# Performance work log

Measured on AMD Instinct MI355X. Metric: run time of the kernel, lower is better.

The kernel has to match this reference:

```python
import jax, jax.numpy as jnp
import numpy as np

N = 20000
F_IN = 500
HID = 64
CLS = 16
H = 4
K_KNN = 10
NEG_SLOPE = 0.2


def _edges(key, n_rand):
    # random edges plus self-loops (mirrors add_self_loops in the torch code)
    src = jax.random.randint(key, (n_rand,), 0, N)
    dst = jax.random.randint(jax.random.fold_in(key, 1), (n_rand,), 0, N)
    loops = jnp.arange(N)
    return jnp.stack([jnp.concatenate([src, loops]), jnp.concatenate([dst, loops])]).astype(jnp.int32)


def setup_inputs():
    key = jax.random.key(0)
    ks = jax.random.split(key, 40)
    inp = {}
    inp['x'] = jax.random.normal(ks[0], (N, F_IN), jnp.float32)
    inp['edge_index_1'] = _edges(ks[1], 16 * N)          # 1-hop graph, 340k edges
    inp['edge_index_2'] = _edges(ks[2], 32 * N)          # denser 2-hop graph, 660k edges
    knn_src = jnp.repeat(jnp.arange(N), K_KNN)
    knn_dst = jax.random.randint(ks[3], (K_KNN * N,), 0, N)
    inp['edge_index_knn'] = jnp.stack([knn_src, knn_dst]).astype(jnp.int32)

    def p(k, shape):
        return jax.random.normal(k, shape, jnp.float32) * 0.05

    dims = {1: (F_IN, HID), 2: (HID, CLS), 3: (F_IN, HID), 4: (HID, CLS), 5: (F_IN, HID), 6: (HID, CLS)}
    i = 4
    for j in range(1, 7):
        fi, fo = dims[j]
        inp[f'W{j}'] = p(ks[i], (fi, H, fo)); i += 1
        inp[f'as{j}'] = p(ks[i], (H, fo)); i += 1
        inp[f'ad{j}'] = p(ks[i], (H, fo)); i += 1
        inp[f'b{j}'] = jnp.zeros((fo,), jnp.float32)
    for j in range(1, 4):
        inp[f'lin{j}_w'] = p(ks[i], (CLS, CLS)); i += 1
        inp[f'lin{j}_b'] = jnp.zeros((CLS,), jnp.float32)
    inp['agg_w'] = p(ks[i], (CLS,))
    return inp


def gat_conv(x, ei, W, a_s, a_d, b):
    # PyG GATConv, concat=False (mean over heads). W: [F,H,D], a_s/a_d: [H,D], b: [D]
    src, dst = ei[0], ei[1]
    z = jnp.einsum('nf,fhd->nhd', x, W)                 # [N,H,D]
    e_src = jnp.sum(z * a_s, -1)                         # [N,H]
    e_dst = jnp.sum(z * a_d, -1)                         # [N,H]
    e = jax.nn.leaky_relu(e_src[src] + e_dst[dst], NEG_SLOPE)   # [E,H]
    m = jax.ops.segment_max(e, dst, num_segments=N)      # per-dst softmax (edge softmax)
    p = jnp.exp(e - m[dst])
    s = jax.ops.segment_sum(p, dst, num_segments=N)
    alpha = p / (s[dst] + 1e-16)                         # [E,H]
    out = jax.ops.segment_sum(alpha[:, :, None] * z[src], dst, num_segments=N)  # [N,H,D]
    return out.mean(1) + b


def reference(x, edge_index_1, edge_index_2, edge_index_knn,
              W1, as1, ad1, b1, W2, as2, ad2, b2,
              W3, as3, ad3, b3, W4, as4, ad4, b4,
              W5, as5, ad5, b5, W6, as6, ad6, b6,
              lin1_w, lin1_b, lin2_w, lin2_b, lin3_w, lin3_b, agg_w):
    # eval mode: dropout is a no-op
    h1 = jax.nn.relu(gat_conv(x, edge_index_1, W1, as1, ad1, b1))
    h1 = gat_conv(h1, edge_index_1, W2, as2, ad2, b2)
    h2 = jax.nn.relu(gat_conv(x, edge_index_2, W3, as3, ad3, b3))
    h2 = gat_conv(h2, edge_index_2, W4, as4, ad4, b4)
    h3 = jax.nn.relu(gat_conv(x, edge_index_knn, W5, as5, ad5, b5))
    h3 = gat_conv(h3, edge_index_knn, W6, as6, ad6, b6)

    a1 = jnp.tanh(h1 @ lin1_w + lin1_b) @ agg_w          # [N]
    a2 = jnp.tanh(h2 @ lin2_w + lin2_b) @ agg_w
    a3 = jnp.tanh(h3 @ lin3_w + lin3_b) @ agg_w
    a = jax.nn.softmax(jnp.stack([a1, a2, a3], axis=1), axis=1)  # [N,3]
    h = a[:, 0:1] * h1 + a[:, 1:2] * h2 + a[:, 2:3] * h3
    return jax.nn.log_softmax(h, axis=1)
```

## Files before the change

kernel.cpp:

```cpp
#include <hip/hip_runtime.h>
#include <hip/hip_bf16.h>
#include <math.h>

#define N_NODES 20000
#define MP      20096
#define FIN     500
#define KP      512
#define NBUCK   157

typedef unsigned short u16;
typedef unsigned char  u8;
typedef __attribute__((ext_vector_type(8))) short   short8;
typedef __attribute__((ext_vector_type(2))) unsigned uv2;
typedef __attribute__((ext_vector_type(2))) float   f32x2;
typedef __attribute__((ext_vector_type(4))) float   f32x4;

__device__ __forceinline__ float b2f(u16 u){
  union { unsigned int i; float f; } v; v.i = ((unsigned int)u) << 16; return v.f;
}
__device__ __forceinline__ u16 f2b(float f){
  __hip_bfloat16 h = __float2bfloat16(f);
  return *reinterpret_cast<u16*>(&h);
}
__device__ __forceinline__ float lrelu(float x){ return x >= 0.f ? x : 0.2f * x; }
__device__ __forceinline__ float ldp(const void* p, int i, int bf){
  return bf ? b2f(((const u16*)p)[i]) : ((const float*)p)[i];
}
__device__ __forceinline__ u8 f2fp8(float f){
  return (u8)(__builtin_amdgcn_cvt_pk_fp8_f32(f, 0.f, 0, false) & 0xff);
}
template<bool HI>
__device__ __forceinline__ f32x2 fp8pair(unsigned w){
  return __builtin_amdgcn_cvt_pk_f32_fp8((int)w, HI);
}
__device__ __forceinline__ void gll16(const u16* g, u16* l){
  __builtin_amdgcn_global_load_lds(
      (const __attribute__((address_space(1))) unsigned int*)g,
      (__attribute__((address_space(3))) unsigned int*)l, 16, 0, 0);
}
__device__ __forceinline__ void barrier_lgkm(){
  asm volatile("s_waitcnt lgkmcnt(0)" ::: "memory");
  __builtin_amdgcn_s_barrier();
  asm volatile("" ::: "memory");
}

__global__ __launch_bounds__(1024) void detect_dtype_kernel(const unsigned int* __restrict__ xw, int nwords,
                                                            int* __restrict__ flag){
  __shared__ int cnt;
  if (threadIdx.x == 0) cnt = 0;
  __syncthreads();
  int c = 0;
  for (int i = threadIdx.x; i < nwords; i += 1024){
    unsigned e = (xw[i] >> 7) & 0xFF;
    if (e >= 0x70 && e <= 0x8F) c++;
  }
  atomicAdd(&cnt, c);
  __syncthreads();
  if (threadIdx.x == 0) *flag = (cnt * 2 > nwords) ? 1 : 0;
}

#define CHA 8192
#define PB  1024
__global__ __launch_bounds__(PB) void prep_kernel(
    const void* __restrict__ x, u16* __restrict__ xp,
    const void* Wb0, const void* Wb1, const void* Wb2,
    const void* Ws0, const void* Ws1, const void* Ws2,
    u16* ob0, u16* ob1, u16* ob2, u16* os0, u16* os1, u16* os2,
    const int* s0, const int* s1, const int* s2,
    const int* d0, const int* d1, const int* d2,
    int E0, int E1, int E2, int S0, int S1, int S2, int EB,
    int* __restrict__ bucketCur, unsigned* p0, unsigned* p1, unsigned* p2,
    const int* __restrict__ flag){
  __shared__ int hb[NBUCK];
  __shared__ int loff[NBUCK];
  __shared__ int hbase[NBUCK];
  __shared__ unsigned shp[CHA];
  __shared__ u8 shb[CHA];
  __shared__ u16 tile[64][65];
  int bf = *flag;
  int tid = threadIdx.x;
  if (blockIdx.y == 0){
    int t = blockIdx.x * PB + tid;
    if (t >= MP * 64) return;
    int row = t >> 6;
    int j0  = (t & 63) * 8;
    short8 v = {0,0,0,0,0,0,0,0};
    if (row < N_NODES){
      if (j0 + 8 <= FIN){
        if (bf){
          const ushort4* xr = (const ushort4*)((const u16*)x + (size_t)row * FIN + j0);
          ushort4 a = xr[0], b = xr[1];
          v[0]=(short)a.x; v[1]=(short)a.y; v[2]=(short)a.z; v[3]=(short)a.w;
          v[4]=(short)b.x; v[5]=(short)b.y; v[6]=(short)b.z; v[7]=(short)b.w;
        } else {
          const float4* xr = (const float4*)((const float*)x + (size_t)row * FIN + j0);
          float4 a = xr[0], b = xr[1];
          v[0]=(short)f2b(a.x); v[1]=(short)f2b(a.y); v[2]=(short)f2b(a.z); v[3]=(short)f2b(a.w);
          v[4]=(short)f2b(b.x); v[5]=(short)f2b(b.y); v[6]=(short)f2b(b.z); v[7]=(short)f2b(b.w);
        }
      } else {
#pragma unroll
        for (int j = 0; j < 8; ++j){
          int k = j0 + j;
          u16 val = 0;
          if (k < FIN)
            val = bf ? ((const u16*)x)[(size_t)row * FIN + k]
                     : f2b(((const float*)x)[(size_t)row * FIN + k]);
          v[j] = (short)val;
        }
      }
    }
    *(short8*)(xp + (size_t)row * KP + j0) = v;
  } else if (blockIdx.y == 1){
    int xb = blockIdx.x;
    if (xb >= 96 + 3) return;
    int tx = tid & 63, tyb = tid >> 6;
    const void* Wsrc; u16* O; int SRCW, SRCH, DSTW, kt, nt;
    if (xb < 96){
      int which = xb >> 5, tl = xb & 31;
      nt = (tl & 3) << 6; kt = (tl >> 2) << 6;
      Wsrc = which == 0 ? Wb0 : (which == 1 ? Wb1 : Wb2);
      O    = which == 0 ? ob0 : (which == 1 ? ob1 : ob2);
      SRCW = 256; SRCH = FIN; DSTW = KP;
    } else {
      int which = xb - 96;
      nt = 0; kt = 0;
      Wsrc = which == 0 ? Ws0 : (which == 1 ? Ws1 : Ws2);
      O    = which == 0 ? os0 : (which == 1 ? os1 : os2);
      SRCW = 64; SRCH = 64; DSTW = 64;
    }
#pragma unroll
    for (int r = 0; r < 4; ++r){
      int kl = tyb + r * 16;
      int k = kt + kl, n = nt + tx;
      u16 vv = 0;
      if (k < SRCH)
        vv = bf ? ((const u16*)Wsrc)[(size_t)k * SRCW + n]
                : f2b(((const float*)Wsrc)[(size_t)k * SRCW + n]);
      tile[kl][tx] = vv;
    }
    __syncthreads();
#pragma unroll
    for (int r = 0; r < 4; ++r){
      int nl = tyb + r * 16;
      O[(size_t)(nt + nl) * DSTW + kt + tx] = tile[tx][nl];
    }
  } else {
    int sblk = blockIdx.x;
    if (sblk >= 3 * EB) return;
    int g = sblk / EB;
    const int* src = g == 0 ? s0 : (g == 1 ? s1 : s2);
    const int* dst = g == 0 ? d0 : (g == 1 ? d1 : d2);
    unsigned* pairs = g == 0 ? p0 : (g == 1 ? p1 : p2);
    int E = g == 0 ? E0 : (g == 1 ? E1 : E2);
    int S = g == 0 ? S0 : (g == 1 ? S1 : S2);
    int base = (sblk % EB) * CHA;
    if (base >= E) return;
    if (tid < NBUCK) hb[tid] = 0;
    __syncthreads();
    constexpr int EPT = CHA / PB;
    int rk[EPT]; unsigned pr[EPT]; int bk[EPT]; bool vl[EPT];
#pragma unroll
    for (int i = 0; i < EPT; ++i){
      int e = base + i * PB + tid;
      vl[i] = e < E;
      bk[i] = 0; rk[i] = 0; pr[i] = 0;
      if (vl[i]){
        int dd = dst[e], ss = src[e];
        bk[i] = dd >> 7;
        pr[i] = ((unsigned)ss << 7) | (unsigned)(dd & 127);
        rk[i] = atomicAdd(&hb[bk[i]], 1);
      }
    }
    __syncthreads();
    int ret = 0;
    if (tid < NBUCK) ret = atomicAdd(&bucketCur[g * NBUCK + tid], hb[tid]);
    if (tid == 0){
      int run = 0;
      for (int k = 0; k < NBUCK; ++k){ loff[k] = run; run += hb[k]; }
    }
    barrier_lgkm();
#pragma unroll
    for (int i = 0; i < EPT; ++i)
      if (vl[i]){
        int j = loff[bk[i]] + rk[i];
        shp[j] = pr[i];
        shb[j] = (u8)bk[i];
      }
    if (tid < NBUCK) hbase[tid] = ret;
    __syncthreads();
    int nb = E - base; if (nb > CHA) nb = CHA;
    for (int j = tid; j < nb; j += PB){
      int b = shb[j];
      int pos = hbase[b] + (j - loff[b]);
      if (pos < S)
        pairs[(size_t)b * S + pos] = shp[j];
    }
  }
}

__global__ __launch_bounds__(1024) void csr_finalize_kernel(
    const unsigned* p0, const unsigned* p1, const unsigned* p2,
    int S0, int S1, int S2,
    const int* __restrict__ bucketCur,
    int* e0, int* e1, int* e2,
    int2* __restrict__ metaB){
  int g = blockIdx.y;
  const unsigned* pairs = g == 0 ? p0 : (g == 1 ? p1 : p2);
  int* esrc = g == 0 ? e0 : (g == 1 ? e1 : e2);
  int S = g == 0 ? S0 : (g == 1 ? S1 : S2);
  int2* meta = metaB + (size_t)g * MP;
  int b = blockIdx.x;
  int nb = bucketCur[g * NBUCK + b];
  if (nb > S) nb = S;
  const unsigned* pb = pairs + (size_t)b * S;
  int* eb = esrc + (size_t)b * S;
  __shared__ int cnt[128];
  __shared__ int loff[128];
  __shared__ int cur[128];
  if (threadIdx.x < 128) cnt[threadIdx.x] = 0;
  __syncthreads();
  for (int i = threadIdx.x; i < nb; i += 1024)
    atomicAdd(&cnt[pb[i] & 127], 1);
  __syncthreads();
  if (threadIdx.x == 0){
    int run = 0;
    for (int k = 0; k < 128; ++k){ loff[k] = run; run += cnt[k]; }
  }
  __syncthreads();
  if (threadIdx.x < 128){
    cur[threadIdx.x] = loff[threadIdx.x];
    int d = b * 128 + threadIdx.x;
    if (d < N_NODES){
      int2 m; m.x = b * S + loff[threadIdx.x]; m.y = cnt[threadIdx.x];
      meta[d] = m;
    }
  }
  __syncthreads();
  for (int i = threadIdx.x; i < nb; i += 1024){
    unsigned u = pb[i];
    int slot = atomicAdd(&cur[u & 127], 1);
    eb[slot] = (int)(u >> 7);
  }
}

__global__ __launch_bounds__(256) void gemm_big_kernel(const u16* __restrict__ A,
    const u16* B0, const u16* B1, const u16* B2,
    u8* C0, u8* C1, u8* C2,
    const void* as0, const void* as1, const void* as2,
    const void* ad0, const void* ad1, const void* ad2,
    float* __restrict__ esB, float* __restrict__ edB,
    const int* __restrict__ flag, int M){
  int g = blockIdx.z;
  const u16* BT = g == 0 ? B0 : (g == 1 ? B1 : B2);
  u8* C = g == 0 ? C0 : (g == 1 ? C1 : C2);
  const void* as_ = g == 0 ? as0 : (g == 1 ? as1 : as2);
  const void* ad_ = g == 0 ? ad0 : (g == 1 ? ad1 : ad2);
  float* es = esB + (size_t)g * N_NODES * 4;
  float* ed = edB + (size_t)g * N_NODES * 4;
  __shared__ alignas(16) u16 As[128 * 64];
  __shared__ alignas(16) u16 Bs[128 * 64];
  const int K = KP, Nn = 256;
  int t = threadIdx.x, lane = t & 63, w = t >> 6;
  int m0 = blockIdx.y * 128, n0 = blockIdx.x * 128;
  int mw = (w >> 1) * 64, nw = (w & 1) * 64;
  f32x4 acc[4][4] = {};
  for (int k0 = 0; k0 < K; k0 += 64){
    __syncthreads();
#pragma unroll
    for (int i = 0; i < 4; ++i){
      int c = i * 256 + w * 64 + lane;
      int row = c >> 3, slot = c & 7;
      int kk = ((slot ^ (row & 7))) * 8;
      gll16(A  + (size_t)(m0 + row) * K + k0 + kk, As + (size_t)(i * 256 + w * 64) * 8);
      gll16(BT + (size_t)(n0 + row) * K + k0 + kk, Bs + (size_t)(i * 256 + w * 64) * 8);
    }
    __syncthreads();
#pragma unroll
    for (int ks = 0; ks < 2; ++ks){
      short8 af[4], bfr[4];
#pragma unroll
      for (int mi = 0; mi < 4; ++mi){
        int row = mw + mi * 16 + (lane & 15);
        int sl = (ks * 4 + (lane >> 4)) ^ (row & 7);
        af[mi] = *(const short8*)(As + (size_t)row * 64 + sl * 8);
      }
#pragma unroll
      for (int ni = 0; ni < 4; ++ni){
        int row = nw + ni * 16 + (lane & 15);
        int sl = (ks * 4 + (lane >> 4)) ^ (row & 7);
        bfr[ni] = *(const short8*)(Bs + (size_t)row * 64 + sl * 8);
      }
#pragma unroll
      for (int mi = 0; mi < 4; ++mi)
#pragma unroll
        for (int ni = 0; ni < 4; ++ni)
          acc[mi][ni] = __builtin_amdgcn_mfma_f32_16x16x32_bf16(af[mi], bfr[ni], acc[mi][ni], 0, 0, 0);
    }
  }
  int bf = *flag;
#pragma unroll
  for (int mi = 0; mi < 4; ++mi)
#pragma unroll
    for (int ni = 0; ni < 4; ++ni)
#pragma unroll
      for (int r = 0; r < 4; ++r){
        int row = m0 + mw + mi * 16 + (lane >> 4) * 4 + r;
        int col = n0 + nw + ni * 16 + (lane & 15);
        if (row < M) C[(size_t)row * Nn + col] = f2fp8(acc[mi][ni][r]);
      }
  {
    int h = (n0 + nw) >> 6;
    float asv[4], adv[4];
#pragma unroll
    for (int ni = 0; ni < 4; ++ni){
      int col = n0 + nw + ni * 16 + (lane & 15);
      asv[ni] = ldp(as_, col, bf);
      adv[ni] = ldp(ad_, col, bf);
    }
#pragma unroll
    for (int mi = 0; mi < 4; ++mi)
#pragma unroll
      for (int r = 0; r < 4; ++r){
        float ps = 0.f, pd2 = 0.f;
#pragma unroll
        for (int ni = 0; ni < 4; ++ni){
          ps  += acc[mi][ni][r] * asv[ni];
          pd2 += acc[mi][ni][r] * adv[ni];
        }
#pragma unroll
        for (int m2 = 1; m2 < 16; m2 <<= 1){
          ps  += __shfl_xor(ps, m2);
          pd2 += __shfl_xor(pd2, m2);
        }
        int row = m0 + mw + mi * 16 + (lane >> 4) * 4 + r;
        if ((lane & 15) == 0 && row < M){
          es[(size_t)row * 4 + h] = ps;
          ed[(size_t)row * 4 + h] = pd2;
        }
      }
  }
}

__global__ __launch_bounds__(256) void gemm_small_kernel(
    const u16* A0, const u16* A1, const u16* A2,
    const u16* B0, const u16* B1, const u16* B2,
    u8* C0, u8* C1, u8* C2,
    const void* as0, const void* as1, const void* as2,
    const void* ad0, const void* ad1, const void* ad2,
    float* __restrict__ esB, float* __restrict__ edB,
    const int* __restrict__ flag, int M){
  int g = blockIdx.y;
  const u16* A  = g == 0 ? A0 : (g == 1 ? A1 : A2);
  const u16* BT = g == 0 ? B0 : (g == 1 ? B1 : B2);
  u8* C = g == 0 ? C0 : (g == 1 ? C1 : C2);
  const void* as_ = g == 0 ? as0 : (g == 1 ? as1 : as2);
  const void* ad_ = g == 0 ? ad0 : (g == 1 ? ad1 : ad2);
  float* es = esB + (size_t)g * N_NODES * 4;
  float* ed = edB + (size_t)g * N_NODES * 4;
  __shared__ alignas(16) u16 As[64 * 64];
  __shared__ alignas(16) u16 Bs[64 * 64];
  int t = threadIdx.x, lane = t & 63, w = t >> 6;
  int m0 = blockIdx.x * 64;
#pragma unroll
  for (int i = 0; i < 2; ++i){
    int c = i * 256 + w * 64 + lane;
    int row = c >> 3, slot = c & 7;
    int kk = ((slot ^ (row & 7))) * 8;
    gll16(A  + (size_t)(m0 + row) * 64 + kk, As + (size_t)(i * 256 + w * 64) * 8);
    gll16(BT + (size_t)row * 64 + kk,        Bs + (size_t)(i * 256 + w * 64) * 8);
  }
  __syncthreads();
  f32x4 acc[4] = {};
  int mw = w * 16;
#pragma unroll
  for (int ks = 0; ks < 2; ++ks){
    int rowa = mw + (lane & 15);
    int sla = (ks * 4 + (lane >> 4)) ^ (rowa & 7);
    short8 af = *(const short8*)(As + (size_t)rowa * 64 + sla * 8);
#pragma unroll
    for (int ni = 0; ni < 4; ++ni){
      int rowb = ni * 16 + (lane & 15);
      int slb = (ks * 4 + (lane >> 4)) ^ (rowb & 7);
      short8 bv = *(const short8*)(Bs + (size_t)rowb * 64 + slb * 8);
      acc[ni] = __builtin_amdgcn_mfma_f32_16x16x32_bf16(af, bv, acc[ni], 0, 0, 0);
    }
  }
  int bf = *flag;
#pragma unroll
  for (int ni = 0; ni < 4; ++ni)
#pragma unroll
    for (int r = 0; r < 4; ++r){
      int row = m0 + mw + (lane >> 4) * 4 + r;
      int col = ni * 16 + (lane & 15);
      if (row < M) C[(size_t)row * 64 + col] = f2fp8(acc[ni][r]);
    }
  {
    float asv[4], adv[4];
#pragma unroll
    for (int ni = 0; ni < 4; ++ni){
      int col = ni * 16 + (lane & 15);
      asv[ni] = ldp(as_, col, bf);
      adv[ni] = ldp(ad_, col, bf);
    }
#pragma unroll
    for (int r = 0; r < 4; ++r){
      float ps[4], pd2[4];
#pragma unroll
      for (int ni = 0; ni < 4; ++ni){ ps[ni] = acc[ni][r] * asv[ni]; pd2[ni] = acc[ni][r] * adv[ni]; }
#pragma unroll
      for (int m2 = 1; m2 < 16; m2 <<= 1)
#pragma unroll
        for (int ni = 0; ni < 4; ++ni){
          ps[ni]  += __shfl_xor(ps[ni], m2);
          pd2[ni] += __shfl_xor(pd2[ni], m2);
        }
      int row = m0 + mw + (lane >> 4) * 4 + r;
      if ((lane & 15) == 0 && row < M){
#pragma unroll
        for (int ni = 0; ni < 4; ++ni){
          es[(size_t)row * 4 + ni] = ps[ni];
          ed[(size_t)row * 4 + ni] = pd2[ni];
        }
      }
    }
  }
}

template<int DT, bool RELU, bool BF16OUT, int PIPE>
__global__ __launch_bounds__(256) void gat_agg5_kernel(
    const u8* z0, const u8* z1, const u8* z2,
    const float* __restrict__ esB, const float* __restrict__ edB,
    const int2* __restrict__ metaB,
    const int* e0p, const int* e1p, const int* e2p,
    const void* b0, const void* b1, const void* b2,
    void* o0, void* o1, void* o2,
    const int* __restrict__ flag){
  int g = blockIdx.y;
  const u8* z = g == 0 ? z0 : (g == 1 ? z1 : z2);
  const int* esrc = g == 0 ? e0p : (g == 1 ? e1p : e2p);
  const void* bias = g == 0 ? b0 : (g == 1 ? b1 : b2);
  void* out = g == 0 ? o0 : (g == 1 ? o1 : o2);
  const float* es = esB + (size_t)g * N_NODES * 4;
  const float* ed = edB + (size_t)g * N_NODES * 4;
  const int2* meta = metaB + (size_t)g * MP;
  int bf = *flag;

  int d = (blockIdx.x * 256 + threadIdx.x) >> 6;
  int lane = threadIdx.x & 63;
  if (d >= N_NODES) return;
  constexpr int LPG = DT / 8;
  constexpr int G   = 64 / LPG;
  constexpr int HD  = DT / 4;
  int grp = lane / LPG;
  int li  = lane % LPG;
  int c0  = li * 8;
  int h   = c0 / HD;

  int2 md = meta[d];
  int deg = md.y;
  const int* ep = esrc + md.x;
  float edh = ed[(unsigned)d * 4 + h];

  float acc[8] = {0,0,0,0,0,0,0,0};
  float sacc = 0.f;

  int steps = (deg + PIPE * G - 1) / (PIPE * G);
  for (int tb = 0; tb < steps; ++tb){
    int e0 = tb * PIPE * G + grp;
    int s[PIPE]; float q[PIPE]; uv2 v[PIPE]; bool val[PIPE];
#pragma unroll
    for (int i = 0; i < PIPE; ++i){
      int e = e0 + i * G;
      val[i] = e < deg;
      int sl = ep[e];
      s[i] = val[i] ? sl : 0;
    }
#pragma unroll
    for (int i = 0; i < PIPE; ++i) q[i] = es[(unsigned)s[i] * 4 + h];
#pragma unroll
    for (int i = 0; i < PIPE; ++i) v[i] = *(const uv2*)(z + (unsigned)s[i] * DT + c0);
#pragma unroll
    for (int i = 0; i < PIPE; ++i){
      float p = val[i] ? __expf(lrelu(q[i] + edh)) : 0.f;
      sacc += p;
      f32x2 a0 = fp8pair<false>(v[i][0]), a1 = fp8pair<true>(v[i][0]);
      f32x2 a2 = fp8pair<false>(v[i][1]), a3 = fp8pair<true>(v[i][1]);
      acc[0] = fmaf(p, a0.x, acc[0]); acc[1] = fmaf(p, a0.y, acc[1]);
      acc[2] = fmaf(p, a1.x, acc[2]); acc[3] = fmaf(p, a1.y, acc[3]);
      acc[4] = fmaf(p, a2.x, acc[4]); acc[5] = fmaf(p, a2.y, acc[5]);
      acc[6] = fmaf(p, a3.x, acc[6]); acc[7] = fmaf(p, a3.y, acc[7]);
    }
  }

#pragma unroll
  for (int m = LPG; m < 64; m <<= 1){
    sacc += __shfl_xor(sacc, m);
#pragma unroll
    for (int j = 0; j < 8; ++j) acc[j] += __shfl_xor(acc[j], m);
  }
  float inv = 1.f / (sacc + 1e-16f);
  float v8[8];
#pragma unroll
  for (int j = 0; j < 8; ++j) v8[j] = acc[j] * inv;
#pragma unroll
  for (int m = HD / 8; m < LPG; m <<= 1)
#pragma unroll
    for (int j = 0; j < 8; ++j) v8[j] += __shfl_xor(v8[j], m);

  if (lane < HD / 8){
    if constexpr (BF16OUT){
      short8 ov;
#pragma unroll
      for (int j = 0; j < 8; ++j){
        float o = v8[j] * 0.25f + ldp(bias, lane * 8 + j, bf);
        if (RELU) o = fmaxf(o, 0.f);
        ov[j] = (short)f2b(o);
      }
      *(short8*)((u16*)out + (size_t)d * HD + lane * 8) = ov;
    } else {
      float o[8];
#pragma unroll
      for (int j = 0; j < 8; ++j){
        o[j] = v8[j] * 0.25f + ldp(bias, lane * 8 + j, bf);
        if (RELU) o[j] = fmaxf(o[j], 0.f);
      }
      float* op = (float*)out + (size_t)d * HD + lane * 8;
      *(float4*)op = make_float4(o[0], o[1], o[2], o[3]);
      *(float4*)(op + 4) = make_float4(o[4], o[5], o[6], o[7]);
    }
  }
}

__global__ __launch_bounds__(256) void final_combine_kernel(
    const float* __restrict__ h1, const float* __restrict__ h2, const float* __restrict__ h3,
    const void* l1w, const void* l1b, const void* l2w, const void* l2b,
    const void* l3w, const void* l3b, const void* aggw,
    void* __restrict__ outv, int n, const int* __restrict__ flag){
  __shared__ float Lw[3][16][16];
  __shared__ float Lb[3][16];
  __shared__ float Ag[16];
  int t = threadIdx.x;
  int bf = *flag;
  {
    const void* ws[3] = { l1w, l2w, l3w };
    for (int g = 0; g < 3; ++g) Lw[g][t / 16][t % 16] = ldp(ws[g], t, bf);
    if (t < 16){
      Lb[0][t] = ldp(l1b, t, bf); Lb[1][t] = ldp(l2b, t, bf); Lb[2][t] = ldp(l3b, t, bf);
      Ag[t] = ldp(aggw, t, bf);
    }
  }
  __syncthreads();
  int node = blockIdx.x * 256 + t;
  if (node >= n) return;
  const float* hp[3] = { h1, h2, h3 };
  float hv[3][16];
  float a[3];
  for (int g = 0; g < 3; ++g){
    const float4* h4 = (const float4*)(hp[g] + (size_t)node * 16);
#pragma unroll
    for (int q = 0; q < 4; ++q){
      float4 f = h4[q];
      hv[g][q * 4 + 0] = f.x; hv[g][q * 4 + 1] = f.y;
      hv[g][q * 4 + 2] = f.z; hv[g][q * 4 + 3] = f.w;
    }
    float dot = 0.f;
#pragma unroll
    for (int j = 0; j < 16; ++j){
      float acc2 = Lb[g][j];
#pragma unroll
      for (int i = 0; i < 16; ++i) acc2 += hv[g][i] * Lw[g][i][j];
      dot += tanhf(acc2) * Ag[j];
    }
    a[g] = dot;
  }
  float am = fmaxf(a[0], fmaxf(a[1], a[2]));
  float e0 = __expf(a[0] - am), e1 = __expf(a[1] - am), e2 = __expf(a[2] - am);
  float einv = 1.f / (e0 + e1 + e2);
  float w0 = e0 * einv, w1 = e1 * einv, w2 = e2 * einv;
  float hh[16];
  float hmax = -INFINITY;
#pragma unroll
  for (int i = 0; i < 16; ++i){
    hh[i] = w0 * hv[0][i] + w1 * hv[1][i] + w2 * hv[2][i];
    hmax = fmaxf(hmax, hh[i]);
  }
  float se = 0.f;
#pragma unroll
  for (int i = 0; i < 16; ++i) se += __expf(hh[i] - hmax);
  float ls = hmax + logf(se);
#pragma unroll
  for (int i = 0; i < 16; ++i){
    float o = hh[i] - ls;
    if (bf) ((__hip_bfloat16*)outv)[(size_t)node * 16 + i] = __float2bfloat16(o);
    else    ((float*)outv)[(size_t)node * 16 + i] = o;
  }
}

extern "C" void kernel_launch(void* const* d_in, const int* in_sizes, int n_in,
                              void* d_out, int out_size, void* d_ws, size_t ws_size,
                              hipStream_t stream){
  const void* x = d_in[0];
  const int* ei[3] = { (const int*)d_in[1], (const int*)d_in[2], (const int*)d_in[3] };
  int E[3] = { in_sizes[1] / 2, in_sizes[2] / 2, in_sizes[3] / 2 };
  int Emax = E[0] > E[1] ? E[0] : E[1]; if (E[2] > Emax) Emax = E[2];
  int EB = (Emax + CHA - 1) / CHA;
  int S[3];
  for (int g = 0; g < 3; ++g){
    long s = ((long)E[g] * 27 / 20) / NBUCK + 64;
    s &= ~63L; if (s > 8192) s = 8192;
    S[g] = (int)s;
  }
  const void *W[6], *as_[6], *ad_[6], *bb[6];
  for (int j = 0; j < 6; ++j){
    W[j]   = d_in[4 + 4 * j];
    as_[j] = d_in[5 + 4 * j];
    ad_[j] = d_in[6 + 4 * j];
    bb[j]  = d_in[7 + 4 * j];
  }
  const void* l1w = d_in[28]; const void* l1b = d_in[29];
  const void* l2w = d_in[30]; const void* l2b = d_in[31];
  const void* l3w = d_in[32]; const void* l3b = d_in[33];
  const void* agg = d_in[34];

  char* p = (char*)d_ws;
  auto alloc = [&](size_t bytes) -> void* {
    void* r = (void*)p;
    p += (bytes + 255) & ~(size_t)255;
    return r;
  };
  int* dflag = (int*)alloc(256);
  u16* xp = (u16*)alloc((size_t)MP * KP * 2);
  u16* hmid[3]; for (int g = 0; g < 3; ++g) hmid[g] = xp + (size_t)g * MP * 64;
  u16* wtb[3]; for (int g = 0; g < 3; ++g) wtb[g] = (u16*)alloc((size_t)256 * KP * 2);
  u16* wts[3]; for (int g = 0; g < 3; ++g) wts[g] = (u16*)alloc((size_t)64 * 64 * 2);
  u8* zf[3];   for (int g = 0; g < 3; ++g) zf[g]  = (u8*)alloc((size_t)N_NODES * 256 + 256);
  float* hbr[3]; for (int g = 0; g < 3; ++g) hbr[g] = (float*)alloc((size_t)N_NODES * 16 * 4);
  float* esB = (float*)alloc((size_t)3 * N_NODES * 4 * 4);
  float* edB = (float*)alloc((size_t)3 * N_NODES * 4 * 4);
  int* bucketCur = (int*)alloc((size_t)3 * NBUCK * 4);
  int2* metaB    = (int2*)alloc((size_t)3 * MP * 8);
  int* esrc[3];
  for (int g = 0; g < 3; ++g) esrc[g] = (int*)alloc(((size_t)NBUCK * S[g] + 256) * 4);
  unsigned* pairs[3];
  for (int g = 0; g < 3; ++g) pairs[g] = (unsigned*)alloc(((size_t)NBUCK * S[g] + 256) * 4);

  const int* s0 = ei[0];          const int* s1 = ei[1];          const int* s2 = ei[2];
  const int* d0 = ei[0] + E[0];   const int* d1 = ei[1] + E[1];   const int* d2 = ei[2] + E[2];

  (void)hipMemsetAsync(bucketCur, 0, (size_t)3 * NBUCK * 4, stream);
  detect_dtype_kernel<<<1, 1024, 0, stream>>>((const unsigned int*)x, 4096, dflag);
  prep_kernel<<<dim3((MP * 64 + PB - 1) / PB, 3), PB, 0, stream>>>(
      x, xp, W[0], W[2], W[4], W[1], W[3], W[5],
      wtb[0], wtb[1], wtb[2], wts[0], wts[1], wts[2],
      s0, s1, s2, d0, d1, d2, E[0], E[1], E[2], S[0], S[1], S[2], EB,
      bucketCur, pairs[0], pairs[1], pairs[2], dflag);
  csr_finalize_kernel<<<dim3(NBUCK, 3), 1024, 0, stream>>>(
      pairs[0], pairs[1], pairs[2], S[0], S[1], S[2], bucketCur,
      esrc[0], esrc[1], esrc[2], metaB);

  const int convGrid = (N_NODES + 3) / 4;

  gemm_big_kernel<<<dim3(2, MP / 128, 3), 256, 0, stream>>>(
      xp, wtb[0], wtb[1], wtb[2], zf[0], zf[1], zf[2],
      as_[0], as_[2], as_[4], ad_[0], ad_[2], ad_[4], esB, edB, dflag, N_NODES);
  gat_agg5_kernel<256, true, true, 6><<<dim3(convGrid, 3), 256, 0, stream>>>(
      zf[0], zf[1], zf[2], esB, edB, metaB, esrc[0], esrc[1], esrc[2],
      bb[0], bb[2], bb[4], (void*)hmid[0], (void*)hmid[1], (void*)hmid[2], dflag);

  gemm_small_kernel<<<dim3(MP / 64, 3), 256, 0, stream>>>(
      hmid[0], hmid[1], hmid[2], wts[0], wts[1], wts[2], zf[0], zf[1], zf[2],
      as_[1], as_[3], as_[5], ad_[1], ad_[3], ad_[5], esB, edB, dflag, N_NODES);
  gat_agg5_kernel<64, false, false, 4><<<dim3(convGrid, 3), 256, 0, stream>>>(
      zf[0], zf[1], zf[2], esB, edB, metaB, esrc[0], esrc[1], esrc[2],
      bb[1], bb[3], bb[5], (void*)hbr[0], (void*)hbr[1], (void*)hbr[2], dflag);

  final_combine_kernel<<<(N_NODES + 255) / 256, 256, 0, stream>>>(
      hbr[0], hbr[1], hbr[2], l1w, l1b, l2w, l2b, l3w, l3b, agg,
      d_out, N_NODES, dflag);
}
```

Measured before the change: 331.2 us.

## Split each destination node's edge list across two wavefronts in GAT aggregation

The aggregation kernel now assigns two wavefronts to each destination node, each handling half the incoming edges, and merges the partial sums through shared memory after a block barrier. The grid becomes a flat 1D launch of 3x10000 blocks with the graph index taken from the block id, and the pipeline depths drop to 5 and 2. This is meant to raise memory-level parallelism and shorten per-node latency chains, at the cost of twice as many waves, an extra LDS round trip and a barrier. It also replaces tanhf in the final combine with an exp-based tanh.

```diff
diff --git a/kernel.cpp b/kernel.cpp
--- a/kernel.cpp
+++ b/kernel.cpp
@@ -7,6 +7,7 @@
 #define FIN     500
 #define KP      512
 #define NBUCK   157
+#define BPG2    10000
 
 typedef unsigned short u16;
 typedef unsigned char  u8;
@@ -42,6 +43,10 @@
   asm volatile("s_waitcnt lgkmcnt(0)" ::: "memory");
   __builtin_amdgcn_s_barrier();
   asm volatile("" ::: "memory");
+}
+__device__ __forceinline__ float ftanh(float x){
+  float ex = __expf(2.f * x);
+  return 1.f - 2.f / (ex + 1.f);
 }
 
 __global__ __launch_bounds__(1024) void detect_dtype_kernel(const unsigned int* __restrict__ xw, int nwords,
@@ -125,7 +130,7 @@
     } else {
       int which = xb - 96;
       nt = 0; kt = 0;
-      Wsrc = which == 0 ? Ws0 : (which == 1 ? Ws1 : Ws2);
+      Wsrc = which == 3 - 3 + 0 ? Ws0 : (which == 1 ? Ws1 : Ws2);
       O    = which == 0 ? os0 : (which == 1 ? os1 : os2);
       SRCW = 64; SRCH = 64; DSTW = 64;
     }
@@ -436,7 +441,9 @@
     const void* b0, const void* b1, const void* b2,
     void* o0, void* o1, void* o2,
     const int* __restrict__ flag){
-  int g = blockIdx.y;
+  int bx = blockIdx.x;
+  int g = bx / BPG2;
+  int blk = bx - g * BPG2;
   const u8* z = g == 0 ? z0 : (g == 1 ? z1 : z2);
   const int* esrc = g == 0 ? e0p : (g == 1 ? e1p : e2p);
   const void* bias = g == 0 ? b0 : (g == 1 ? b1 : b2);
@@ -446,9 +453,11 @@
   const int2* meta = metaB + (size_t)g * MP;
   int bf = *flag;
 
-  int d = (blockIdx.x * 256 + threadIdx.x) >> 6;
+  int w    = threadIdx.x >> 6;
+  int pair = w >> 1;
+  int half = w & 1;
+  int d    = blk * 2 + pair;
   int lane = threadIdx.x & 63;
-  if (d >= N_NODES) return;
   constexpr int LPG = DT / 8;
   constexpr int G   = 64 / LPG;
   constexpr int HD  = DT / 4;
@@ -459,20 +468,23 @@
 
   int2 md = meta[d];
   int deg = md.y;
-  const int* ep = esrc + md.x;
+  int mid = deg >> 1;
+  int start = half ? mid : 0;
+  int dloc  = half ? (deg - mid) : mid;
+  const int* ep = esrc + md.x + start;
   float edh = ed[(unsigned)d * 4 + h];
 
   float acc[8] = {0,0,0,0,0,0,0,0};
   float sacc = 0.f;
 
-  int steps = (deg + PIPE * G - 1) / (PIPE * G);
+  int steps = (dloc + PIPE * G - 1) / (PIPE * G);
   for (int tb = 0; tb < steps; ++tb){
     int e0 = tb * PIPE * G + grp;
     int s[PIPE]; float q[PIPE]; uv2 v[PIPE]; bool val[PIPE];
 #pragma unroll
     for (int i = 0; i < PIPE; ++i){
       int e = e0 + i * G;
-      val[i] = e < deg;
+      val[i] = e < dloc;
       int sl = ep[e];
       s[i] = val[i] ? sl : 0;
     }
@@ -491,6 +503,22 @@
       acc[4] = fmaf(p, a2.x, acc[4]); acc[5] = fmaf(p, a2.y, acc[5]);
       acc[6] = fmaf(p, a3.x, acc[6]); acc[7] = fmaf(p, a3.y, acc[7]);
     }
+  }
+
+  __shared__ float comb[2][64][9];
+  if (half){
+    float* c = &comb[pair][lane][0];
+#pragma unroll
+    for (int j = 0; j < 8; ++j) c[j] = acc[j];
+    c[8] = sacc;
+  }
+  __syncthreads();
+  if (half) return;
+  {
+    const float* c = &comb[pair][lane][0];
+#pragma unroll
+    for (int j = 0; j < 8; ++j) acc[j] += c[j];
+    sacc += c[8];
   }
 
 #pragma unroll
@@ -570,7 +598,7 @@
       float acc2 = Lb[g][j];
 #pragma unroll
       for (int i = 0; i < 16; ++i) acc2 += hv[g][i] * Lw[g][i][j];
-      dot += tanhf(acc2) * Ag[j];
+      dot += ftanh(acc2) * Ag[j];
     }
     a[g] = dot;
   }
@@ -659,19 +687,17 @@
       pairs[0], pairs[1], pairs[2], S[0], S[1], S[2], bucketCur,
       esrc[0], esrc[1], esrc[2], metaB);
 
-  const int convGrid = (N_NODES + 3) / 4;
-
   gemm_big_kernel<<<dim3(2, MP / 128, 3), 256, 0, stream>>>(
       xp, wtb[0], wtb[1], wtb[2], zf[0], zf[1], zf[2],
       as_[0], as_[2], as_[4], ad_[0], ad_[2], ad_[4], esB, edB, dflag, N_NODES);
-  gat_agg5_kernel<256, true, true, 6><<<dim3(convGrid, 3), 256, 0, stream>>>(
+  gat_agg5_kernel<256, true, true, 5><<<dim3(3 * BPG2), 256, 0, stream>>>(
       zf[0], zf[1], zf[2], esB, edB, metaB, esrc[0], esrc[1], esrc[2],
       bb[0], bb[2], bb[4], (void*)hmid[0], (void*)hmid[1], (void*)hmid[2], dflag);
 
   gemm_small_kernel<<<dim3(MP / 64, 3), 256, 0, stream>>>(
       hmid[0], hmid[1], hmid[2], wts[0], wts[1], wts[2], zf[0], zf[1], zf[2],
       as_[1], as_[3], as_[5], ad_[1], ad_[3], ad_[5], esB, edB, dflag, N_NODES);
-  gat_agg5_kernel<64, false, false, 4><<<dim3(convGrid, 3), 256, 0, stream>>>(
+  gat_agg5_kernel<64, false, false, 2><<<dim3(3 * BPG2), 256, 0, stream>>>(
       zf[0], zf[1], zf[2], esB, edB, metaB, esrc[0], esrc[1], esrc[2],
       bb[1], bb[3], bb[5], (void*)hbr[0], (void*)hbr[1], (void*)hbr[2], dflag);
 
```

Measured after the change: 345.3 us. 4.3% more time.

## Fuse CSR finalize into big GEMM launch and regroup GEMM tiles for reuse

Applied to the files above, without the earlier changes.

The CSR finalize work now runs as extra blocks (blockIdx.z==1) inside the big GEMM launch, removing one kernel launch and letting the edge sorting overlap with the GEMM. The GEMM grid is remapped to 1D with groups of 8 M-tiles times 6 (graph, N-half) combos, so that blocks sharing A rows run close together for L2 reuse. The final combine also swaps tanhf for an exp-based tanh. The finalize blocks now use 256 threads instead of 1024, and the fast tanh gives up a little accuracy.

```diff
diff --git a/kernel.cpp b/kernel.cpp
--- a/kernel.cpp
+++ b/kernel.cpp
@@ -42,6 +42,10 @@
   asm volatile("s_waitcnt lgkmcnt(0)" ::: "memory");
   __builtin_amdgcn_s_barrier();
   asm volatile("" ::: "memory");
+}
+__device__ __forceinline__ float ftanh(float x){
+  float ex = __expf(2.f * x);
+  return 1.f - 2.f / (ex + 1.f);
 }
 
 __global__ __launch_bounds__(1024) void detect_dtype_kernel(const unsigned int* __restrict__ xw, int nwords,
@@ -199,70 +203,76 @@
   }
 }
 
-__global__ __launch_bounds__(1024) void csr_finalize_kernel(
-    const unsigned* p0, const unsigned* p1, const unsigned* p2,
-    int S0, int S1, int S2,
-    const int* __restrict__ bucketCur,
-    int* e0, int* e1, int* e2,
-    int2* __restrict__ metaB){
-  int g = blockIdx.y;
-  const unsigned* pairs = g == 0 ? p0 : (g == 1 ? p1 : p2);
-  int* esrc = g == 0 ? e0 : (g == 1 ? e1 : e2);
-  int S = g == 0 ? S0 : (g == 1 ? S1 : S2);
-  int2* meta = metaB + (size_t)g * MP;
-  int b = blockIdx.x;
-  int nb = bucketCur[g * NBUCK + b];
-  if (nb > S) nb = S;
-  const unsigned* pb = pairs + (size_t)b * S;
-  int* eb = esrc + (size_t)b * S;
-  __shared__ int cnt[128];
-  __shared__ int loff[128];
-  __shared__ int cur[128];
-  if (threadIdx.x < 128) cnt[threadIdx.x] = 0;
-  __syncthreads();
-  for (int i = threadIdx.x; i < nb; i += 1024)
-    atomicAdd(&cnt[pb[i] & 127], 1);
-  __syncthreads();
-  if (threadIdx.x == 0){
-    int run = 0;
-    for (int k = 0; k < 128; ++k){ loff[k] = run; run += cnt[k]; }
-  }
-  __syncthreads();
-  if (threadIdx.x < 128){
-    cur[threadIdx.x] = loff[threadIdx.x];
-    int d = b * 128 + threadIdx.x;
-    if (d < N_NODES){
-      int2 m; m.x = b * S + loff[threadIdx.x]; m.y = cnt[threadIdx.x];
-      meta[d] = m;
-    }
-  }
-  __syncthreads();
-  for (int i = threadIdx.x; i < nb; i += 1024){
-    unsigned u = pb[i];
-    int slot = atomicAdd(&cur[u & 127], 1);
-    eb[slot] = (int)(u >> 7);
-  }
-}
-
 __global__ __launch_bounds__(256) void gemm_big_kernel(const u16* __restrict__ A,
     const u16* B0, const u16* B1, const u16* B2,
     u8* C0, u8* C1, u8* C2,
     const void* as0, const void* as1, const void* as2,
     const void* ad0, const void* ad1, const void* ad2,
     float* __restrict__ esB, float* __restrict__ edB,
-    const int* __restrict__ flag, int M){
-  int g = blockIdx.z;
+    const int* __restrict__ flag, int M,
+    const unsigned* p0, const unsigned* p1, const unsigned* p2,
+    int S0, int S1, int S2, const int* __restrict__ bucketCur,
+    int* e0, int* e1, int* e2, int2* __restrict__ metaB){
+  __shared__ alignas(16) u16 As[128 * 64];
+  __shared__ alignas(16) u16 Bs[128 * 64];
+  __shared__ int ccnt[128];
+  __shared__ int cloff[128];
+  __shared__ int ccur[128];
+  int t = threadIdx.x;
+  if (blockIdx.z == 1){
+    int bxc = blockIdx.x;
+    if (bxc >= 3 * NBUCK) return;
+    int g = bxc / NBUCK, b = bxc - g * NBUCK;
+    const unsigned* pairs = g == 0 ? p0 : (g == 1 ? p1 : p2);
+    int* esrc = g == 0 ? e0 : (g == 1 ? e1 : e2);
+    int S = g == 0 ? S0 : (g == 1 ? S1 : S2);
+    int2* meta = metaB + (size_t)g * MP;
+    int nb = bucketCur[g * NBUCK + b];
+    if (nb > S) nb = S;
+    const unsigned* pb = pairs + (size_t)b * S;
+    int* eb = esrc + (size_t)b * S;
+    if (t < 128) ccnt[t] = 0;
+    __syncthreads();
+    for (int i = t; i < nb; i += 256)
+      atomicAdd(&ccnt[pb[i] & 127], 1);
+    __syncthreads();
+    if (t == 0){
+      int run = 0;
+      for (int k = 0; k < 128; ++k){ cloff[k] = run; run += ccnt[k]; }
+    }
+    __syncthreads();
+    if (t < 128){
+      ccur[t] = cloff[t];
+      int d = b * 128 + t;
+      if (d < N_NODES){
+        int2 m; m.x = b * S + cloff[t]; m.y = ccnt[t];
+        meta[d] = m;
+      }
+    }
+    __syncthreads();
+    for (int i = t; i < nb; i += 256){
+      unsigned u = pb[i];
+      int slot = atomicAdd(&ccur[u & 127], 1);
+      eb[slot] = (int)(u >> 7);
+    }
+    return;
+  }
+  int bx = blockIdx.x;
+  int grp = bx / 48, j = bx - grp * 48;
+  int ng = j >> 3, sub = j & 7;
+  int mt = grp * 8 + sub;
+  if (mt >= MP / 128) return;
+  int g  = ng >> 1;
+  int n0 = (ng & 1) * 128;
+  int m0 = mt * 128;
   const u16* BT = g == 0 ? B0 : (g == 1 ? B1 : B2);
   u8* C = g == 0 ? C0 : (g == 1 ? C1 : C2);
   const void* as_ = g == 0 ? as0 : (g == 1 ? as1 : as2);
   const void* ad_ = g == 0 ? ad0 : (g == 1 ? ad1 : ad2);
   float* es = esB + (size_t)g * N_NODES * 4;
   float* ed = edB + (size_t)g * N_NODES * 4;
-  __shared__ alignas(16) u16 As[128 * 64];
-  __shared__ alignas(16) u16 Bs[128 * 64];
   const int K = KP, Nn = 256;
-  int t = threadIdx.x, lane = t & 63, w = t >> 6;
-  int m0 = blockIdx.y * 128, n0 = blockIdx.x * 128;
+  int lane = t & 63, w = t >> 6;
   int mw = (w >> 1) * 64, nw = (w & 1) * 64;
   f32x4 acc[4][4] = {};
   for (int k0 = 0; k0 < K; k0 += 64){
@@ -570,7 +580,7 @@
       float acc2 = Lb[g][j];
 #pragma unroll
       for (int i = 0; i < 16; ++i) acc2 += hv[g][i] * Lw[g][i][j];
-      dot += tanhf(acc2) * Ag[j];
+      dot += ftanh(acc2) * Ag[j];
     }
     a[g] = dot;
   }
@@ -655,15 +665,14 @@
       wtb[0], wtb[1], wtb[2], wts[0], wts[1], wts[2],
       s0, s1, s2, d0, d1, d2, E[0], E[1], E[2], S[0], S[1], S[2], EB,
       bucketCur, pairs[0], pairs[1], pairs[2], dflag);
-  csr_finalize_kernel<<<dim3(NBUCK, 3), 1024, 0, stream>>>(
+
+  const int convGrid = (N_NODES + 3) / 4;
+
+  gemm_big_kernel<<<dim3(20 * 48, 1, 2), 256, 0, stream>>>(
+      xp, wtb[0], wtb[1], wtb[2], zf[0], zf[1], zf[2],
+      as_[0], as_[2], as_[4], ad_[0], ad_[2], ad_[4], esB, edB, dflag, N_NODES,
       pairs[0], pairs[1], pairs[2], S[0], S[1], S[2], bucketCur,
       esrc[0], esrc[1], esrc[2], metaB);
-
-  const int convGrid = (N_NODES + 3) / 4;
-
-  gemm_big_kernel<<<dim3(2, MP / 128, 3), 256, 0, stream>>>(
-      xp, wtb[0], wtb[1], wtb[2], zf[0], zf[1], zf[2],
-      as_[0], as_[2], as_[4], ad_[0], ad_[2], ad_[4], esB, edB, dflag, N_NODES);
   gat_agg5_kernel<256, true, true, 6><<<dim3(convGrid, 3), 256, 0, stream>>>(
       zf[0], zf[1], zf[2], esB, edB, metaB, esrc[0], esrc[1], esrc[2],
       bb[0], bb[2], bb[4], (void*)hmid[0], (void*)hmid[1], (void*)hmid[2], dflag);
```

Measured after the change: 323.7 us. 1.02x faster.
